# Kernel optimization log

Measured on AMD Instinct MI355X. Metric: run time of the kernel, lower is better.

Reference implementation:

```python
import jax, jax.numpy as jnp
import numpy as np

N, E, M = 100000, 1600000, 10000
D_IN, D_HID, D_OUT = 128, 128, 128


def setup_inputs() -> dict:
    key = jax.random.key(0)
    ks = jax.random.split(key, 16)
    feat = jax.random.normal(ks[0], (N, D_IN), dtype=jnp.float32)
    src = jax.random.randint(ks[1], (E,), 0, N, dtype=jnp.int32)
    dst = jax.random.randint(ks[2], (E,), 0, N, dtype=jnp.int32)
    masked_offset = jax.random.randint(ks[3], (M,), 0, N, dtype=jnp.int32)
    def xavier(k, shape):
        fan_in, fan_out = shape[0], shape[1]
        a = jnp.sqrt(6.0 / (fan_in + fan_out))
        return jax.random.uniform(k, shape, jnp.float32, -a, a)
    return {
        'feat': feat, 'src': src, 'dst': dst, 'masked_offset': masked_offset,
        # GraphConv layers (weight [in,out], bias [out])
        'W1': xavier(ks[4], (D_IN, D_HID)), 'b1': jnp.zeros((D_HID,), jnp.float32),
        'W2': xavier(ks[5], (D_HID, D_HID)), 'b2': jnp.zeros((D_HID,), jnp.float32),
        # fusion MLP
        'Wm1': xavier(ks[6], (D_HID + D_IN, D_HID)), 'bm1': jnp.zeros((D_HID,), jnp.float32),
        'Wm2': xavier(ks[7], (D_HID, D_HID)), 'bm2': jnp.zeros((D_HID,), jnp.float32),
        'Wm3': xavier(ks[8], (D_HID, D_OUT)),  # final Linear has bias=False
    }


def _graph_conv_right(h, src, dst, W, b, inv_deg):
    # DGL GraphConv(norm='right'): aggregate src features at dst, divide by in-degree.
    # Apply weight first (in_feats >= out_feats path) -- mathematically identical.
    hw = h @ W                                   # [N, out]
    agg = jax.ops.segment_sum(hw[src], dst, num_segments=N)  # scatter-add over edges
    return agg * inv_deg + b


def reference(feat, src, dst, masked_offset, W1, b1, W2, b2, Wm1, bm1, Wm2, bm2, Wm3):
    ones = jnp.ones((E,), jnp.float32)
    deg = jax.ops.segment_sum(ones, dst, num_segments=N)
    inv_deg = (1.0 / jnp.clip(deg, 1.0, None))[:, None]      # [N,1]
    # GCN layer 1 + ReLU (Identity norm)
    h = jax.nn.relu(_graph_conv_right(feat, src, dst, W1, b1, inv_deg))
    # GCN layer 2 (last layer: no activation; dropout no-op at eval)
    h = _graph_conv_right(h, src, dst, W2, b2, inv_deg)
    # fusion == 'cat': relu(Identity(h[masked])) concat raw features
    hm = jax.nn.relu(h[masked_offset])                       # [M, H]
    x = jnp.concatenate([hm, feat[masked_offset]], axis=1)   # [M, H+D]
    x = jax.nn.relu(x @ Wm1 + bm1)
    x = jax.nn.relu(x @ Wm2 + bm2)
    return x @ Wm3
```

## Files before the change

### kernel.cpp

```cpp
#include <hip/hip_runtime.h>

#define NN 100000
#define NE 1600000
#define NM 10000
#define NSB 256
#define SUBN 391
#define CAP2 7424
#define PCH 2048

typedef __attribute__((ext_vector_type(8))) short bf16x8;
typedef __attribute__((ext_vector_type(4))) float f32x4;

__device__ inline float4 ld4(const float* p) { return *(const float4*)p; }
__device__ inline float bf2f(unsigned short u) {
  union { unsigned int i; float f; } c; c.i = ((unsigned int)u) << 16; return c.f;
}
__device__ inline unsigned short f2bf(float f) {
  union { float f; unsigned int i; } c; c.f = f;
  unsigned int u = c.i + 0x7fffu + ((c.i >> 16) & 1u);
  return (unsigned short)(u >> 16);
}

__global__ __launch_bounds__(256) void part2_k(const int* __restrict__ src,
                                               const int* __restrict__ dst,
                                               unsigned* __restrict__ parts2,
                                               int* __restrict__ pcnt2) {
  __shared__ int cntw[4][NSB];
  __shared__ int basew[4][NSB];
  __shared__ int bstart[NSB + 1];
  __shared__ int gbase[NSB];
  __shared__ int wsum[4];
  __shared__ unsigned buf[PCH];
  const int tid = threadIdx.x;
  const int wv = tid >> 6;
  const int e0 = blockIdx.x * PCH;

  for (int i = tid; i < 4 * NSB; i += 256) ((int*)cntw)[i] = 0;
  __syncthreads();

  unsigned pk[8];
  int b_[8], lp_[8];
#pragma unroll
  for (int j = 0; j < 8; ++j) {
    int e = e0 + j * 256 + tid;
    bool ok = e < NE;
    int s = ok ? src[e] : 0;
    int d = ok ? dst[e] : 0;
    int b = d / SUBN;
    int ld = d - b * SUBN;
    pk[j] = ((unsigned)ld << 17) | (unsigned)s;
    b_[j] = ok ? b : -1;
    if (ok) lp_[j] = atomicAdd(&cntw[wv][b], 1);
  }
  __syncthreads();
  int t0 = cntw[0][tid], t1 = cntw[1][tid], t2 = cntw[2][tid], t3 = cntw[3][tid];
  int tot = t0 + t1 + t2 + t3;
  int x = tot;
#pragma unroll
  for (int d = 1; d < 64; d <<= 1) {
    int y = __shfl_up(x, d, 64);
    if ((tid & 63) >= d) x += y;
  }
  if ((tid & 63) == 63) wsum[wv] = x;
  __syncthreads();
  int woff = 0;
#pragma unroll
  for (int w = 0; w < 4; ++w) woff += (w < wv) ? wsum[w] : 0;
  int excl = x + woff - tot;
  bstart[tid] = excl;
  basew[0][tid] = excl;
  basew[1][tid] = excl + t0;
  basew[2][tid] = excl + t0 + t1;
  basew[3][tid] = excl + t0 + t1 + t2;
  gbase[tid] = atomicAdd(&pcnt2[tid], tot);
  if (tid == NSB - 1) bstart[NSB] = excl + tot;
  __syncthreads();
#pragma unroll
  for (int j = 0; j < 8; ++j)
    if (b_[j] >= 0) buf[basew[wv][b_[j]] + lp_[j]] = pk[j];
  __syncthreads();
  int total = bstart[NSB];
  for (int i = tid; i < total; i += 256) {
    int lo = 0, hi = NSB;
    while (hi - lo > 1) { int mid = (lo + hi) >> 1; if (bstart[mid] <= i) lo = mid; else hi = mid; }
    int gi = gbase[lo] + (i - bstart[lo]);
    if (gi < CAP2) parts2[(size_t)lo * CAP2 + gi] = buf[i];
  }
}

__global__ __launch_bounds__(1024) void deg2_k(const unsigned* __restrict__ parts2,
                                               const int* __restrict__ pcnt2,
                                               int* __restrict__ deg) {
  __shared__ int cnt[SUBN];
  int sb = blockIdx.x;
  int n = min(pcnt2[sb], CAP2);
  const unsigned* p = parts2 + (size_t)sb * CAP2;
  for (int i = threadIdx.x; i < SUBN; i += 1024) cnt[i] = 0;
  __syncthreads();
  for (int i = threadIdx.x; i < n; i += 1024) atomicAdd(&cnt[p[i] >> 17], 1);
  __syncthreads();
  int base = sb * SUBN;
  for (int i = threadIdx.x; i < SUBN; i += 1024)
    if (base + i < NN) deg[base + i] = cnt[i];
}

__global__ __launch_bounds__(1024) void scan1_k(const int* __restrict__ deg,
                                                int* __restrict__ excl,
                                                int* __restrict__ bsum, int n) {
  __shared__ int lds[1024];
  int tid = threadIdx.x;
  int gid = blockIdx.x * 1024 + tid;
  int v = (gid < n) ? deg[gid] : 0;
  lds[tid] = v;
  __syncthreads();
  for (int off = 1; off < 1024; off <<= 1) {
    int t = (tid >= off) ? lds[tid - off] : 0;
    __syncthreads();
    lds[tid] += t;
    __syncthreads();
  }
  if (gid < n) excl[gid] = lds[tid] - v;
  if (tid == 1023) bsum[blockIdx.x] = lds[1023];
}

__global__ void scan2_k(int* __restrict__ bsum, int nb) {
  __shared__ int lds[128];
  int tid = threadIdx.x;
  int v = (tid < nb) ? bsum[tid] : 0;
  lds[tid] = v;
  __syncthreads();
  for (int off = 1; off < 128; off <<= 1) {
    int t = (tid >= off) ? lds[tid - off] : 0;
    __syncthreads();
    lds[tid] += t;
    __syncthreads();
  }
  if (tid < nb) bsum[tid] = lds[tid] - v;
}

__global__ __launch_bounds__(256) void scan3_k(int* __restrict__ excl,
                                               const int* __restrict__ bsum,
                                               const int* __restrict__ deg,
                                               float* __restrict__ inv, int n) {
  int gid = blockIdx.x * 256 + threadIdx.x;
  if (gid < n) {
    excl[gid] += bsum[gid >> 10] + deg[gid];
    inv[gid] = 1.0f / fmaxf((float)deg[gid], 1.0f);
  }
}

__global__ __launch_bounds__(1024) void sort_emit_k(const unsigned* __restrict__ parts2,
                                                    const int* __restrict__ pcnt2,
                                                    const int* __restrict__ offs_end,
                                                    const int* __restrict__ degv,
                                                    int* __restrict__ csr) {
  __shared__ int cur[SUBN];
  __shared__ int sorted[CAP2];
  int sb = blockIdx.x;
  int n = min(pcnt2[sb], CAP2);
  const unsigned* p = parts2 + (size_t)sb * CAP2;
  int base = sb * SUBN;
  int segbase = offs_end[base] - degv[base];
  for (int i = threadIdx.x; i < SUBN; i += 1024) {
    int nd = base + i;
    cur[i] = (nd < NN) ? (offs_end[nd] - degv[nd]) : 0;
  }
  __syncthreads();
  for (int i = threadIdx.x; i < n; i += 1024) {
    unsigned v = p[i];
    int pos = atomicAdd(&cur[v >> 17], 1);
    sorted[pos - segbase] = (int)(v & 0x1FFFFu);
  }
  __syncthreads();
  for (int i = threadIdx.x; i < n; i += 1024) csr[segbase + i] = sorted[i];
}

__global__ __launch_bounds__(256) void tobf_k(const float* __restrict__ x,
                                              unsigned short* __restrict__ y, int n) {
  int idx = (blockIdx.x * 256 + threadIdx.x) * 4;
  if (idx < n) {
    float4 v = ld4(x + idx);
    unsigned int lo = (unsigned int)f2bf(v.x) | ((unsigned int)f2bf(v.y) << 16);
    unsigned int hi = (unsigned int)f2bf(v.z) | ((unsigned int)f2bf(v.w) << 16);
    *(uint2*)(y + idx) = make_uint2(lo, hi);
  }
}

__device__ inline void conv4(const float* s, unsigned short* d, int q) {
  float4 v = ld4(s + q * 4);
  unsigned int lo = (unsigned int)f2bf(v.x) | ((unsigned int)f2bf(v.y) << 16);
  unsigned int hi = (unsigned int)f2bf(v.z) | ((unsigned int)f2bf(v.w) << 16);
  ((uint2*)d)[q] = make_uint2(lo, hi);
}
__global__ __launch_bounds__(256) void wconv_k(const float* W1, const float* W2,
                                               const float* Wm1, const float* Wm2,
                                               const float* Wm3,
                                               unsigned short* W1bf, unsigned short* W2bf,
                                               unsigned short* Wm1bf, unsigned short* Wm2bf,
                                               unsigned short* Wm3bf) {
  int q = blockIdx.x * 256 + threadIdx.x;
  if (q < 4096) conv4(W1, W1bf, q);
  else if (q < 8192) conv4(W2, W2bf, q - 4096);
  else if (q < 16384) conv4(Wm1, Wm1bf, q - 8192);
  else if (q < 20480) conv4(Wm2, Wm2bf, q - 16384);
  else if (q < 24576) conv4(Wm3, Wm3bf, q - 20480);
}

__global__ __launch_bounds__(256) void gather1_k(const unsigned short* __restrict__ featbf,
                                                 const int* __restrict__ csr,
                                                 const int* __restrict__ offs_end,
                                                 const int* __restrict__ degv,
                                                 const float* __restrict__ inv,
                                                 unsigned short* __restrict__ agg1) {
  int v = blockIdx.x * 8 + (threadIdx.x >> 5);
  if (v >= NN) return;
  int lane = threadIdx.x & 31;
  int cnt = degv[v];
  int start = offs_end[v] - cnt;
  const uint2* fb = (const uint2*)featbf;
  float a0 = 0.f, a1 = 0.f, a2 = 0.f, a3 = 0.f;
  int nb8 = (cnt + 7) >> 3;
  for (int it = 0; it < nb8; ++it) {
    int b = start + (it << 3);
    int rem = cnt - (it << 3);
    int sidx[8]; float msk[8];
#pragma unroll
    for (int j = 0; j < 8; ++j) {
      bool ok = j < rem;
      sidx[j] = csr[b + (ok ? j : 0)];
      msk[j] = ok ? 1.f : 0.f;
    }
    uint2 x[8];
#pragma unroll
    for (int j = 0; j < 8; ++j) x[j] = fb[(size_t)sidx[j] * 32 + lane];
#pragma unroll
    for (int j = 0; j < 8; ++j) {
      a0 = fmaf(msk[j], bf2f((unsigned short)(x[j].x)), a0);
      a1 = fmaf(msk[j], bf2f((unsigned short)(x[j].x >> 16)), a1);
      a2 = fmaf(msk[j], bf2f((unsigned short)(x[j].y)), a2);
      a3 = fmaf(msk[j], bf2f((unsigned short)(x[j].y >> 16)), a3);
    }
  }
  float iv = inv[v];
  unsigned int lo = (unsigned int)f2bf(a0 * iv) | ((unsigned int)f2bf(a1 * iv) << 16);
  unsigned int hi = (unsigned int)f2bf(a2 * iv) | ((unsigned int)f2bf(a3 * iv) << 16);
  ((uint2*)agg1)[(size_t)v * 32 + lane] = make_uint2(lo, hi);
}

__global__ __launch_bounds__(256) void gather2_k(const unsigned short* __restrict__ h1bf,
                                                 const unsigned short* __restrict__ featbf,
                                                 const int* __restrict__ masked,
                                                 const int* __restrict__ csr,
                                                 const int* __restrict__ offs_end,
                                                 const int* __restrict__ degv,
                                                 const float* __restrict__ inv,
                                                 unsigned short* __restrict__ agg2bf,
                                                 unsigned short* __restrict__ xcatbf) {
  int m = blockIdx.x * 8 + (threadIdx.x >> 5);
  if (m >= NM) return;
  int lane = threadIdx.x & 31;
  int v = masked[m];
  int cnt = degv[v];
  int start = offs_end[v] - cnt;
  const uint2* fb = (const uint2*)h1bf;
  float a0 = 0.f, a1 = 0.f, a2 = 0.f, a3 = 0.f;
  int nb8 = (cnt + 7) >> 3;
  for (int it = 0; it < nb8; ++it) {
    int b = start + (it << 3);
    int rem = cnt - (it << 3);
    int sidx[8]; float msk[8];
#pragma unroll
    for (int j = 0; j < 8; ++j) {
      bool ok = j < rem;
      sidx[j] = csr[b + (ok ? j : 0)];
      msk[j] = ok ? 1.f : 0.f;
    }
    uint2 x[8];
#pragma unroll
    for (int j = 0; j < 8; ++j) x[j] = fb[(size_t)sidx[j] * 32 + lane];
#pragma unroll
    for (int j = 0; j < 8; ++j) {
      a0 = fmaf(msk[j], bf2f((unsigned short)(x[j].x)), a0);
      a1 = fmaf(msk[j], bf2f((unsigned short)(x[j].x >> 16)), a1);
      a2 = fmaf(msk[j], bf2f((unsigned short)(x[j].y)), a2);
      a3 = fmaf(msk[j], bf2f((unsigned short)(x[j].y >> 16)), a3);
    }
  }
  float iv = inv[v];
  unsigned int lo = (unsigned int)f2bf(a0 * iv) | ((unsigned int)f2bf(a1 * iv) << 16);
  unsigned int hi = (unsigned int)f2bf(a2 * iv) | ((unsigned int)f2bf(a3 * iv) << 16);
  ((uint2*)agg2bf)[(size_t)m * 32 + lane] = make_uint2(lo, hi);
  ((uint2*)xcatbf)[(size_t)m * 64 + 32 + lane] = ((const uint2*)featbf)[(size_t)v * 32 + lane];
}

template<int KT, bool BIAS, bool RELU, bool F32OUT>
__global__ __launch_bounds__(256) void mfma_gemm_k(const unsigned short* __restrict__ Abf,
                                                   const unsigned short* __restrict__ Wbf,
                                                   const float* __restrict__ bias,
                                                   void* __restrict__ Yout,
                                                   int ldy, int nrows) {
  const int lda = KT * 32;
  const int tid = threadIdx.x;
  const int wave = tid >> 6;
  const int lane = tid & 63;
  const int l15 = lane & 15;
  const int l4 = lane >> 4;
  const int rbase = blockIdx.x * 64;

  bf16x8 Bfr[2][KT];
#pragma unroll
  for (int c = 0; c < 2; ++c) {
    int col = (wave + 4 * c) * 16 + l15;
#pragma unroll
    for (int kt = 0; kt < KT; ++kt) {
      bf16x8 b;
#pragma unroll
      for (int i = 0; i < 8; ++i)
        b[i] = (short)Wbf[(kt * 32 + l4 * 8 + i) * 128 + col];
      Bfr[c][kt] = b;
    }
  }
  float bias0 = 0.f, bias1 = 0.f;
  if (BIAS) { bias0 = bias[wave * 16 + l15]; bias1 = bias[(wave + 4) * 16 + l15]; }

  for (int rsub = 0; rsub < 4; ++rsub) {
    int arow = rbase + rsub * 16 + l15;
    const unsigned short* ap = Abf + (size_t)(arow < nrows ? arow : 0) * lda;
    f32x4 acc0 = {0.f, 0.f, 0.f, 0.f};
    f32x4 acc1 = {0.f, 0.f, 0.f, 0.f};
#pragma unroll
    for (int kt = 0; kt < KT; ++kt) {
      bf16x8 a = *(const bf16x8*)(ap + kt * 32 + l4 * 8);
      acc0 = __builtin_amdgcn_mfma_f32_16x16x32_bf16(a, Bfr[0][kt], acc0, 0, 0, 0);
      acc1 = __builtin_amdgcn_mfma_f32_16x16x32_bf16(a, Bfr[1][kt], acc1, 0, 0, 0);
    }
#pragma unroll
    for (int r = 0; r < 4; ++r) {
      int orow = rbase + rsub * 16 + l4 * 4 + r;
      if (orow < nrows) {
        float v0 = acc0[r] + bias0, v1 = acc1[r] + bias1;
        if (RELU) { v0 = fmaxf(v0, 0.f); v1 = fmaxf(v1, 0.f); }
        if (F32OUT) {
          ((float*)Yout)[(size_t)orow * ldy + wave * 16 + l15] = v0;
          ((float*)Yout)[(size_t)orow * ldy + (wave + 4) * 16 + l15] = v1;
        } else {
          ((unsigned short*)Yout)[(size_t)orow * ldy + wave * 16 + l15] = f2bf(v0);
          ((unsigned short*)Yout)[(size_t)orow * ldy + (wave + 4) * 16 + l15] = f2bf(v1);
        }
      }
    }
  }
}

extern "C" void kernel_launch(void* const* d_in, const int* in_sizes, int n_in,
                              void* d_out, int out_size, void* d_ws, size_t ws_size,
                              hipStream_t stream) {
  const float* feat = (const float*)d_in[0];
  const int* src = (const int*)d_in[1];
  const int* dst = (const int*)d_in[2];
  const int* masked = (const int*)d_in[3];
  const float* W1 = (const float*)d_in[4];
  const float* b1 = (const float*)d_in[5];
  const float* W2 = (const float*)d_in[6];
  const float* b2 = (const float*)d_in[7];
  const float* Wm1 = (const float*)d_in[8];
  const float* bm1 = (const float*)d_in[9];
  const float* Wm2 = (const float*)d_in[10];
  const float* bm2 = (const float*)d_in[11];
  const float* Wm3 = (const float*)d_in[12];
  float* out = (float*)d_out;

  char* p = (char*)d_ws;
  int* deg = (int*)p;              p += (size_t)NN * 4;
  int* offs = (int*)p;             p += (size_t)NN * 4;
  int* bsum = (int*)p;             p += 128 * 4;
  int* pcnt2 = (int*)p;            p += NSB * 4;
  float* inv = (float*)p;          p += (size_t)NN * 4;
  int* csr = (int*)p;              p += (size_t)NE * 4;
  p = (char*)(((size_t)p + 15) & ~(size_t)15);
  unsigned* parts2 = (unsigned*)p; p += (size_t)NSB * CAP2 * 4;
  p = (char*)(((size_t)p + 15) & ~(size_t)15);
  unsigned short* featbf = (unsigned short*)p;  p += (size_t)NN * 128 * 2;
  unsigned short* agg1 = (unsigned short*)p;    p += (size_t)NN * 128 * 2;
  unsigned short* h1bf = (unsigned short*)p;    p += (size_t)NN * 128 * 2;
  unsigned short* W1bf = (unsigned short*)p;    p += 16384 * 2;
  unsigned short* W2bf = (unsigned short*)p;    p += 16384 * 2;
  unsigned short* Wm1bf = (unsigned short*)p;   p += 32768 * 2;
  unsigned short* Wm2bf = (unsigned short*)p;   p += 16384 * 2;
  unsigned short* Wm3bf = (unsigned short*)p;   p += 16384 * 2;
  p = (char*)(((size_t)p + 15) & ~(size_t)15);
  unsigned short* agg2bf = (unsigned short*)p;  p += (size_t)NM * 128 * 2;
  unsigned short* xcatbf = (unsigned short*)p;  p += (size_t)NM * 256 * 2;
  unsigned short* y1bf = (unsigned short*)p;    p += (size_t)NM * 128 * 2;
  unsigned short* y2bf = (unsigned short*)p;    p += (size_t)NM * 128 * 2;

  (void)hipMemsetAsync(pcnt2, 0, NSB * 4, stream);

  part2_k<<<(NE + PCH - 1) / PCH, 256, 0, stream>>>(src, dst, parts2, pcnt2);
  deg2_k<<<NSB, 1024, 0, stream>>>(parts2, pcnt2, deg);
  int nb = (NN + 1023) / 1024;
  scan1_k<<<nb, 1024, 0, stream>>>(deg, offs, bsum, NN);
  scan2_k<<<1, 128, 0, stream>>>(bsum, nb);
  scan3_k<<<(NN + 255) / 256, 256, 0, stream>>>(offs, bsum, deg, inv, NN);
  sort_emit_k<<<NSB, 1024, 0, stream>>>(parts2, pcnt2, offs, deg, csr);

  tobf_k<<<(NN * 128 / 4 + 255) / 256, 256, 0, stream>>>(feat, featbf, NN * 128);
  wconv_k<<<96, 256, 0, stream>>>(W1, W2, Wm1, Wm2, Wm3, W1bf, W2bf, Wm1bf, Wm2bf, Wm3bf);

  gather1_k<<<(NN + 7) / 8, 256, 0, stream>>>(featbf, csr, offs, deg, inv, agg1);
  mfma_gemm_k<4, true, true, false><<<(NN + 63) / 64, 256, 0, stream>>>(agg1, W1bf, b1, h1bf, 128, NN);

  gather2_k<<<(NM + 7) / 8, 256, 0, stream>>>(h1bf, featbf, masked, csr, offs, deg, inv, agg2bf, xcatbf);
  int gm = (NM + 63) / 64;
  mfma_gemm_k<4, true, true, false><<<gm, 256, 0, stream>>>(agg2bf, W2bf, b2, xcatbf, 256, NM);

  mfma_gemm_k<8, true, true, false><<<gm, 256, 0, stream>>>(xcatbf, Wm1bf, bm1, y1bf, 128, NM);
  mfma_gemm_k<4, true, true, false><<<gm, 256, 0, stream>>>(y1bf, Wm2bf, bm2, y2bf, 128, NM);
  mfma_gemm_k<4, false, false, true><<<gm, 256, 0, stream>>>(y2bf, Wm3bf, nullptr, out, 128, NM);
}
```

Before: 181.4 us.

## Skip unneeded layer-1 nodes, fuse gather+GEMM, fuse MLP chain into one kernel

Result: faster. 175.1 us (-3.5%).

```diff
diff --git a/kernel.cpp b/kernel.cpp
--- a/kernel.cpp
+++ b/kernel.cpp
@@ -19,6 +19,15 @@
   union { float f; unsigned int i; } c; c.f = f;
   unsigned int u = c.i + 0x7fffu + ((c.i >> 16) & 1u);
   return (unsigned short)(u >> 16);
+}
+__device__ inline void stx(unsigned char* base, int rowBytes, int row, int col,
+                           unsigned short val) {
+  int bc = col * 2;
+  int c = bc >> 4, cp = c ^ (row & 15);
+  *(unsigned short*)&base[row * rowBytes + (cp << 4) + (bc & 15)] = val;
+}
+__device__ inline bf16x8 ldx8(const unsigned char* base, int rowBytes, int row, int kc) {
+  return *(const bf16x8*)&base[row * rowBytes + ((kc ^ (row & 15)) << 4)];
 }
 
 __global__ __launch_bounds__(256) void part2_k(const int* __restrict__ src,
@@ -31,6 +40,7 @@
   __shared__ int gbase[NSB];
   __shared__ int wsum[4];
   __shared__ unsigned buf[PCH];
+  __shared__ unsigned char bb[PCH];
   const int tid = threadIdx.x;
   const int wv = tid >> 6;
   const int e0 = blockIdx.x * PCH;
@@ -77,14 +87,17 @@
   __syncthreads();
 #pragma unroll
   for (int j = 0; j < 8; ++j)
-    if (b_[j] >= 0) buf[basew[wv][b_[j]] + lp_[j]] = pk[j];
+    if (b_[j] >= 0) {
+      int pos = basew[wv][b_[j]] + lp_[j];
+      buf[pos] = pk[j];
+      bb[pos] = (unsigned char)b_[j];
+    }
   __syncthreads();
   int total = bstart[NSB];
   for (int i = tid; i < total; i += 256) {
-    int lo = 0, hi = NSB;
-    while (hi - lo > 1) { int mid = (lo + hi) >> 1; if (bstart[mid] <= i) lo = mid; else hi = mid; }
-    int gi = gbase[lo] + (i - bstart[lo]);
-    if (gi < CAP2) parts2[(size_t)lo * CAP2 + gi] = buf[i];
+    int b = bb[i];
+    int gi = gbase[b] + (i - bstart[b]);
+    if (gi < CAP2) parts2[(size_t)b * CAP2 + gi] = buf[i];
   }
 }
 
@@ -186,76 +199,128 @@
   }
 }
 
-__device__ inline void conv4(const float* s, unsigned short* d, int q) {
-  float4 v = ld4(s + q * 4);
-  unsigned int lo = (unsigned int)f2bf(v.x) | ((unsigned int)f2bf(v.y) << 16);
-  unsigned int hi = (unsigned int)f2bf(v.z) | ((unsigned int)f2bf(v.w) << 16);
-  ((uint2*)d)[q] = make_uint2(lo, hi);
+__device__ inline void convfrag(const float* W, unsigned short* Wf, int g) {
+  int k8 = (g >> 7) << 3, col = g & 127;
+  unsigned short tmp[8];
+#pragma unroll
+  for (int i = 0; i < 8; ++i) tmp[i] = f2bf(W[(k8 + i) * 128 + col]);
+  *(uint4*)&Wf[(size_t)g * 8] = *(const uint4*)tmp;
 }
 __global__ __launch_bounds__(256) void wconv_k(const float* W1, const float* W2,
                                                const float* Wm1, const float* Wm2,
                                                const float* Wm3,
-                                               unsigned short* W1bf, unsigned short* W2bf,
-                                               unsigned short* Wm1bf, unsigned short* Wm2bf,
-                                               unsigned short* Wm3bf) {
-  int q = blockIdx.x * 256 + threadIdx.x;
-  if (q < 4096) conv4(W1, W1bf, q);
-  else if (q < 8192) conv4(W2, W2bf, q - 4096);
-  else if (q < 16384) conv4(Wm1, Wm1bf, q - 8192);
-  else if (q < 20480) conv4(Wm2, Wm2bf, q - 16384);
-  else if (q < 24576) conv4(Wm3, Wm3bf, q - 20480);
-}
-
-__global__ __launch_bounds__(256) void gather1_k(const unsigned short* __restrict__ featbf,
-                                                 const int* __restrict__ csr,
-                                                 const int* __restrict__ offs_end,
-                                                 const int* __restrict__ degv,
-                                                 const float* __restrict__ inv,
-                                                 unsigned short* __restrict__ agg1) {
-  int v = blockIdx.x * 8 + (threadIdx.x >> 5);
-  if (v >= NN) return;
+                                               unsigned short* W1f, unsigned short* W2f,
+                                               unsigned short* Wm1f, unsigned short* Wm2f,
+                                               unsigned short* Wm3f) {
+  int g = blockIdx.x * 256 + threadIdx.x;
+  if (g < 2048) convfrag(W1, W1f, g);
+  else if (g < 4096) convfrag(W2, W2f, g - 2048);
+  else if (g < 8192) convfrag(Wm1, Wm1f, g - 4096);
+  else if (g < 10240) convfrag(Wm2, Wm2f, g - 8192);
+  else if (g < 12288) convfrag(Wm3, Wm3f, g - 10240);
+}
+
+__global__ __launch_bounds__(256) void mark_k(const int* __restrict__ masked,
+                                              const int* __restrict__ csr,
+                                              const int* __restrict__ offs_end,
+                                              const int* __restrict__ degv,
+                                              unsigned char* __restrict__ needed) {
+  int m = blockIdx.x * 8 + (threadIdx.x >> 5);
+  if (m >= NM) return;
   int lane = threadIdx.x & 31;
+  int v = masked[m];
   int cnt = degv[v];
   int start = offs_end[v] - cnt;
-  const uint2* fb = (const uint2*)featbf;
-  float a0 = 0.f, a1 = 0.f, a2 = 0.f, a3 = 0.f;
-  int nb8 = (cnt + 7) >> 3;
-  for (int it = 0; it < nb8; ++it) {
-    int b = start + (it << 3);
-    int rem = cnt - (it << 3);
-    int sidx[8]; float msk[8];
-#pragma unroll
-    for (int j = 0; j < 8; ++j) {
-      bool ok = j < rem;
-      sidx[j] = csr[b + (ok ? j : 0)];
-      msk[j] = ok ? 1.f : 0.f;
-    }
-    uint2 x[8];
-#pragma unroll
-    for (int j = 0; j < 8; ++j) x[j] = fb[(size_t)sidx[j] * 32 + lane];
-#pragma unroll
-    for (int j = 0; j < 8; ++j) {
-      a0 = fmaf(msk[j], bf2f((unsigned short)(x[j].x)), a0);
-      a1 = fmaf(msk[j], bf2f((unsigned short)(x[j].x >> 16)), a1);
-      a2 = fmaf(msk[j], bf2f((unsigned short)(x[j].y)), a2);
-      a3 = fmaf(msk[j], bf2f((unsigned short)(x[j].y >> 16)), a3);
-    }
-  }
-  float iv = inv[v];
-  unsigned int lo = (unsigned int)f2bf(a0 * iv) | ((unsigned int)f2bf(a1 * iv) << 16);
-  unsigned int hi = (unsigned int)f2bf(a2 * iv) | ((unsigned int)f2bf(a3 * iv) << 16);
-  ((uint2*)agg1)[(size_t)v * 32 + lane] = make_uint2(lo, hi);
+  for (int i = lane; i < cnt; i += 32) needed[csr[start + i]] = 1;
+}
+
+__global__ __launch_bounds__(256) void fused_l1_k(const unsigned short* __restrict__ featbf,
+                                                  const int* __restrict__ csr,
+                                                  const int* __restrict__ offs_end,
+                                                  const int* __restrict__ degv,
+                                                  const float* __restrict__ inv,
+                                                  const unsigned char* __restrict__ needed,
+                                                  const unsigned short* __restrict__ W1f,
+                                                  const float* __restrict__ b1,
+                                                  unsigned short* __restrict__ h1bf) {
+  __shared__ unsigned char lds[64 * 256];
+  const int tid = threadIdx.x;
+  const int rbase = blockIdx.x * 64;
+  {
+    int grp = tid >> 5, lane = tid & 31;
+    const uint2* fb = (const uint2*)featbf;
+    int c = lane >> 1;
+    for (int k = 0; k < 8; ++k) {
+      int row = grp * 8 + k;
+      int v = rbase + row;
+      unsigned char* dstp = &lds[row * 256 + (((c ^ (row & 15)) << 4)) + (lane & 1) * 8];
+      if (v >= NN || !needed[v]) { *(uint2*)dstp = make_uint2(0u, 0u); continue; }
+      int cnt = degv[v];
+      int start = offs_end[v] - cnt;
+      float a0 = 0.f, a1 = 0.f, a2 = 0.f, a3 = 0.f;
+      int nb8 = (cnt + 7) >> 3;
+      for (int it = 0; it < nb8; ++it) {
+        int b = start + (it << 3);
+        int rem = cnt - (it << 3);
+        int sidx[8]; float msk[8];
+#pragma unroll
+        for (int j = 0; j < 8; ++j) {
+          bool ok = j < rem;
+          sidx[j] = csr[b + (ok ? j : 0)];
+          msk[j] = ok ? 1.f : 0.f;
+        }
+        uint2 x[8];
+#pragma unroll
+        for (int j = 0; j < 8; ++j) x[j] = fb[(size_t)sidx[j] * 32 + lane];
+#pragma unroll
+        for (int j = 0; j < 8; ++j) {
+          a0 = fmaf(msk[j], bf2f((unsigned short)(x[j].x)), a0);
+          a1 = fmaf(msk[j], bf2f((unsigned short)(x[j].x >> 16)), a1);
+          a2 = fmaf(msk[j], bf2f((unsigned short)(x[j].y)), a2);
+          a3 = fmaf(msk[j], bf2f((unsigned short)(x[j].y >> 16)), a3);
+        }
+      }
+      float iv = inv[v];
+      unsigned int lo = (unsigned int)f2bf(a0 * iv) | ((unsigned int)f2bf(a1 * iv) << 16);
+      unsigned int hi = (unsigned int)f2bf(a2 * iv) | ((unsigned int)f2bf(a3 * iv) << 16);
+      *(uint2*)dstp = make_uint2(lo, hi);
+    }
+  }
+  __syncthreads();
+  const int wave = tid >> 6, lane = tid & 63, l15 = lane & 15, l4 = lane >> 4;
+  int col0 = wave * 16 + l15, col1 = (wave + 4) * 16 + l15;
+  float bias0 = b1[col0], bias1 = b1[col1];
+  for (int rsub = 0; rsub < 4; ++rsub) {
+    int row = rsub * 16 + l15;
+    f32x4 acc0 = {0.f, 0.f, 0.f, 0.f};
+    f32x4 acc1 = {0.f, 0.f, 0.f, 0.f};
+#pragma unroll
+    for (int kt = 0; kt < 4; ++kt) {
+      int kc = kt * 4 + l4;
+      bf16x8 a = ldx8(lds, 256, row, kc);
+      bf16x8 b0 = *(const bf16x8*)&W1f[((size_t)kc * 128 + col0) * 8];
+      bf16x8 b1v = *(const bf16x8*)&W1f[((size_t)kc * 128 + col1) * 8];
+      acc0 = __builtin_amdgcn_mfma_f32_16x16x32_bf16(a, b0, acc0, 0, 0, 0);
+      acc1 = __builtin_amdgcn_mfma_f32_16x16x32_bf16(a, b1v, acc1, 0, 0, 0);
+    }
+#pragma unroll
+    for (int r = 0; r < 4; ++r) {
+      int orow = rbase + rsub * 16 + l4 * 4 + r;
+      if (orow < NN) {
+        h1bf[(size_t)orow * 128 + col0] = f2bf(fmaxf(acc0[r] + bias0, 0.f));
+        h1bf[(size_t)orow * 128 + col1] = f2bf(fmaxf(acc1[r] + bias1, 0.f));
+      }
+    }
+  }
 }
 
 __global__ __launch_bounds__(256) void gather2_k(const unsigned short* __restrict__ h1bf,
-                                                 const unsigned short* __restrict__ featbf,
                                                  const int* __restrict__ masked,
                                                  const int* __restrict__ csr,
                                                  const int* __restrict__ offs_end,
                                                  const int* __restrict__ degv,
                                                  const float* __restrict__ inv,
-                                                 unsigned short* __restrict__ agg2bf,
-                                                 unsigned short* __restrict__ xcatbf) {
+                                                 unsigned short* __restrict__ agg2bf) {
   int m = blockIdx.x * 8 + (threadIdx.x >> 5);
   if (m >= NM) return;
   int lane = threadIdx.x & 31;
@@ -290,62 +355,140 @@
   unsigned int lo = (unsigned int)f2bf(a0 * iv) | ((unsigned int)f2bf(a1 * iv) << 16);
   unsigned int hi = (unsigned int)f2bf(a2 * iv) | ((unsigned int)f2bf(a3 * iv) << 16);
   ((uint2*)agg2bf)[(size_t)m * 32 + lane] = make_uint2(lo, hi);
-  ((uint2*)xcatbf)[(size_t)m * 64 + 32 + lane] = ((const uint2*)featbf)[(size_t)v * 32 + lane];
-}
-
-template<int KT, bool BIAS, bool RELU, bool F32OUT>
-__global__ __launch_bounds__(256) void mfma_gemm_k(const unsigned short* __restrict__ Abf,
-                                                   const unsigned short* __restrict__ Wbf,
-                                                   const float* __restrict__ bias,
-                                                   void* __restrict__ Yout,
-                                                   int ldy, int nrows) {
-  const int lda = KT * 32;
+}
+
+__global__ __launch_bounds__(256) void mlp_fused_k(const unsigned short* __restrict__ agg2bf,
+                                                   const unsigned short* __restrict__ featbf,
+                                                   const int* __restrict__ masked,
+                                                   const unsigned short* __restrict__ W2f,
+                                                   const float* __restrict__ b2,
+                                                   const unsigned short* __restrict__ Wm1f,
+                                                   const float* __restrict__ bm1,
+                                                   const unsigned short* __restrict__ Wm2f,
+                                                   const float* __restrict__ bm2,
+                                                   const unsigned short* __restrict__ Wm3f,
+                                                   float* __restrict__ out) {
+  __shared__ unsigned char ldsX[64 * 512];
+  __shared__ unsigned char ldsY[64 * 256];
   const int tid = threadIdx.x;
-  const int wave = tid >> 6;
-  const int lane = tid & 63;
-  const int l15 = lane & 15;
-  const int l4 = lane >> 4;
   const int rbase = blockIdx.x * 64;
-
-  bf16x8 Bfr[2][KT];
-#pragma unroll
-  for (int c = 0; c < 2; ++c) {
-    int col = (wave + 4 * c) * 16 + l15;
-#pragma unroll
-    for (int kt = 0; kt < KT; ++kt) {
-      bf16x8 b;
-#pragma unroll
-      for (int i = 0; i < 8; ++i)
-        b[i] = (short)Wbf[(kt * 32 + l4 * 8 + i) * 128 + col];
-      Bfr[c][kt] = b;
-    }
-  }
-  float bias0 = 0.f, bias1 = 0.f;
-  if (BIAS) { bias0 = bias[wave * 16 + l15]; bias1 = bias[(wave + 4) * 16 + l15]; }
-
-  for (int rsub = 0; rsub < 4; ++rsub) {
-    int arow = rbase + rsub * 16 + l15;
-    const unsigned short* ap = Abf + (size_t)(arow < nrows ? arow : 0) * lda;
-    f32x4 acc0 = {0.f, 0.f, 0.f, 0.f};
-    f32x4 acc1 = {0.f, 0.f, 0.f, 0.f};
-#pragma unroll
-    for (int kt = 0; kt < KT; ++kt) {
-      bf16x8 a = *(const bf16x8*)(ap + kt * 32 + l4 * 8);
-      acc0 = __builtin_amdgcn_mfma_f32_16x16x32_bf16(a, Bfr[0][kt], acc0, 0, 0, 0);
-      acc1 = __builtin_amdgcn_mfma_f32_16x16x32_bf16(a, Bfr[1][kt], acc1, 0, 0, 0);
-    }
-#pragma unroll
-    for (int r = 0; r < 4; ++r) {
-      int orow = rbase + rsub * 16 + l4 * 4 + r;
-      if (orow < nrows) {
-        float v0 = acc0[r] + bias0, v1 = acc1[r] + bias1;
-        if (RELU) { v0 = fmaxf(v0, 0.f); v1 = fmaxf(v1, 0.f); }
-        if (F32OUT) {
-          ((float*)Yout)[(size_t)orow * ldy + wave * 16 + l15] = v0;
-          ((float*)Yout)[(size_t)orow * ldy + (wave + 4) * 16 + l15] = v1;
-        } else {
-          ((unsigned short*)Yout)[(size_t)orow * ldy + wave * 16 + l15] = f2bf(v0);
-          ((unsigned short*)Yout)[(size_t)orow * ldy + (wave + 4) * 16 + l15] = f2bf(v1);
+  const int wave = tid >> 6, lane = tid & 63, l15 = lane & 15, l4 = lane >> 4;
+  {
+    int grp = tid >> 5, ln = tid & 31;
+    uint2 vals[8];
+#pragma unroll
+    for (int k = 0; k < 8; ++k) {
+      int m = rbase + grp * 8 + k;
+      vals[k] = make_uint2(0u, 0u);
+      if (m < NM) {
+        int v = masked[m];
+        vals[k] = ((const uint2*)featbf)[(size_t)v * 32 + ln];
+      }
+    }
+#pragma unroll
+    for (int k = 0; k < 8; ++k) {
+      int row = grp * 8 + k;
+      int c = 16 + (ln >> 1);
+      *(uint2*)&ldsX[row * 512 + ((c ^ (row & 15)) << 4) + (ln & 1) * 8] = vals[k];
+    }
+  }
+  {
+    int col0 = wave * 16 + l15, col1 = (wave + 4) * 16 + l15;
+    float bias0 = b2[col0], bias1 = b2[col1];
+    for (int rsub = 0; rsub < 4; ++rsub) {
+      int arow = rbase + rsub * 16 + l15;
+      const unsigned short* ap = agg2bf + (size_t)min(arow, NM - 1) * 128;
+      f32x4 acc0 = {0.f, 0.f, 0.f, 0.f};
+      f32x4 acc1 = {0.f, 0.f, 0.f, 0.f};
+#pragma unroll
+      for (int kt = 0; kt < 4; ++kt) {
+        int kc = kt * 4 + l4;
+        bf16x8 a = *(const bf16x8*)(ap + kc * 8);
+        bf16x8 b0 = *(const bf16x8*)&W2f[((size_t)kc * 128 + col0) * 8];
+        bf16x8 b1v = *(const bf16x8*)&W2f[((size_t)kc * 128 + col1) * 8];
+        acc0 = __builtin_amdgcn_mfma_f32_16x16x32_bf16(a, b0, acc0, 0, 0, 0);
+        acc1 = __builtin_amdgcn_mfma_f32_16x16x32_bf16(a, b1v, acc1, 0, 0, 0);
+      }
+#pragma unroll
+      for (int r = 0; r < 4; ++r) {
+        int row = rsub * 16 + l4 * 4 + r;
+        stx(ldsX, 512, row, col0, f2bf(fmaxf(acc0[r] + bias0, 0.f)));
+        stx(ldsX, 512, row, col1, f2bf(fmaxf(acc1[r] + bias1, 0.f)));
+      }
+    }
+  }
+  __syncthreads();
+  {
+    int col0 = wave * 16 + l15, col1 = (wave + 4) * 16 + l15;
+    float bias0 = bm1[col0], bias1 = bm1[col1];
+    for (int rsub = 0; rsub < 4; ++rsub) {
+      int row = rsub * 16 + l15;
+      f32x4 acc0 = {0.f, 0.f, 0.f, 0.f};
+      f32x4 acc1 = {0.f, 0.f, 0.f, 0.f};
+#pragma unroll
+      for (int kt = 0; kt < 8; ++kt) {
+        int kc = kt * 4 + l4;
+        bf16x8 a = ldx8(ldsX, 512, row, kc);
+        bf16x8 b0 = *(const bf16x8*)&Wm1f[((size_t)kc * 128 + col0) * 8];
+        bf16x8 b1v = *(const bf16x8*)&Wm1f[((size_t)kc * 128 + col1) * 8];
+        acc0 = __builtin_amdgcn_mfma_f32_16x16x32_bf16(a, b0, acc0, 0, 0, 0);
+        acc1 = __builtin_amdgcn_mfma_f32_16x16x32_bf16(a, b1v, acc1, 0, 0, 0);
+      }
+#pragma unroll
+      for (int r = 0; r < 4; ++r) {
+        int row2 = rsub * 16 + l4 * 4 + r;
+        stx(ldsY, 256, row2, col0, f2bf(fmaxf(acc0[r] + bias0, 0.f)));
+        stx(ldsY, 256, row2, col1, f2bf(fmaxf(acc1[r] + bias1, 0.f)));
+      }
+    }
+  }
+  __syncthreads();
+  {
+    int col0 = wave * 16 + l15, col1 = (wave + 4) * 16 + l15;
+    float bias0 = bm2[col0], bias1 = bm2[col1];
+    for (int rsub = 0; rsub < 4; ++rsub) {
+      int row = rsub * 16 + l15;
+      f32x4 acc0 = {0.f, 0.f, 0.f, 0.f};
+      f32x4 acc1 = {0.f, 0.f, 0.f, 0.f};
+#pragma unroll
+      for (int kt = 0; kt < 4; ++kt) {
+        int kc = kt * 4 + l4;
+        bf16x8 a = ldx8(ldsY, 256, row, kc);
+        bf16x8 b0 = *(const bf16x8*)&Wm2f[((size_t)kc * 128 + col0) * 8];
+        bf16x8 b1v = *(const bf16x8*)&Wm2f[((size_t)kc * 128 + col1) * 8];
+        acc0 = __builtin_amdgcn_mfma_f32_16x16x32_bf16(a, b0, acc0, 0, 0, 0);
+        acc1 = __builtin_amdgcn_mfma_f32_16x16x32_bf16(a, b1v, acc1, 0, 0, 0);
+      }
+#pragma unroll
+      for (int r = 0; r < 4; ++r) {
+        int row2 = rsub * 16 + l4 * 4 + r;
+        stx(ldsX, 256, row2, col0, f2bf(fmaxf(acc0[r] + bias0, 0.f)));
+        stx(ldsX, 256, row2, col1, f2bf(fmaxf(acc1[r] + bias1, 0.f)));
+      }
+    }
+  }
+  __syncthreads();
+  {
+    int col0 = wave * 16 + l15, col1 = (wave + 4) * 16 + l15;
+    for (int rsub = 0; rsub < 4; ++rsub) {
+      int row = rsub * 16 + l15;
+      f32x4 acc0 = {0.f, 0.f, 0.f, 0.f};
+      f32x4 acc1 = {0.f, 0.f, 0.f, 0.f};
+#pragma unroll
+      for (int kt = 0; kt < 4; ++kt) {
+        int kc = kt * 4 + l4;
+        bf16x8 a = ldx8(ldsX, 256, row, kc);
+        bf16x8 b0 = *(const bf16x8*)&Wm3f[((size_t)kc * 128 + col0) * 8];
+        bf16x8 b1v = *(const bf16x8*)&Wm3f[((size_t)kc * 128 + col1) * 8];
+        acc0 = __builtin_amdgcn_mfma_f32_16x16x32_bf16(a, b0, acc0, 0, 0, 0);
+        acc1 = __builtin_amdgcn_mfma_f32_16x16x32_bf16(a, b1v, acc1, 0, 0, 0);
+      }
+#pragma unroll
+      for (int r = 0; r < 4; ++r) {
+        int orow = rbase + rsub * 16 + l4 * 4 + r;
+        if (orow < NM) {
+          out[(size_t)orow * 128 + col0] = acc0[r];
+          out[(size_t)orow * 128 + col1] = acc1[r];
         }
       }
     }
@@ -377,24 +520,20 @@
   int* pcnt2 = (int*)p;            p += NSB * 4;
   float* inv = (float*)p;          p += (size_t)NN * 4;
   int* csr = (int*)p;              p += (size_t)NE * 4;
+  unsigned char* needed = (unsigned char*)p; p += (size_t)NN;
   p = (char*)(((size_t)p + 15) & ~(size_t)15);
   unsigned* parts2 = (unsigned*)p; p += (size_t)NSB * CAP2 * 4;
-  p = (char*)(((size_t)p + 15) & ~(size_t)15);
   unsigned short* featbf = (unsigned short*)p;  p += (size_t)NN * 128 * 2;
-  unsigned short* agg1 = (unsigned short*)p;    p += (size_t)NN * 128 * 2;
   unsigned short* h1bf = (unsigned short*)p;    p += (size_t)NN * 128 * 2;
-  unsigned short* W1bf = (unsigned short*)p;    p += 16384 * 2;
-  unsigned short* W2bf = (unsigned short*)p;    p += 16384 * 2;
-  unsigned short* Wm1bf = (unsigned short*)p;   p += 32768 * 2;
-  unsigned short* Wm2bf = (unsigned short*)p;   p += 16384 * 2;
-  unsigned short* Wm3bf = (unsigned short*)p;   p += 16384 * 2;
-  p = (char*)(((size_t)p + 15) & ~(size_t)15);
   unsigned short* agg2bf = (unsigned short*)p;  p += (size_t)NM * 128 * 2;
-  unsigned short* xcatbf = (unsigned short*)p;  p += (size_t)NM * 256 * 2;
-  unsigned short* y1bf = (unsigned short*)p;    p += (size_t)NM * 128 * 2;
-  unsigned short* y2bf = (unsigned short*)p;    p += (size_t)NM * 128 * 2;
+  unsigned short* W1f = (unsigned short*)p;     p += 16384 * 2;
+  unsigned short* W2f = (unsigned short*)p;     p += 16384 * 2;
+  unsigned short* Wm1f = (unsigned short*)p;    p += 32768 * 2;
+  unsigned short* Wm2f = (unsigned short*)p;    p += 16384 * 2;
+  unsigned short* Wm3f = (unsigned short*)p;    p += 16384 * 2;
 
   (void)hipMemsetAsync(pcnt2, 0, NSB * 4, stream);
+  (void)hipMemsetAsync(needed, 0, NN, stream);
 
   part2_k<<<(NE + PCH - 1) / PCH, 256, 0, stream>>>(src, dst, parts2, pcnt2);
   deg2_k<<<NSB, 1024, 0, stream>>>(parts2, pcnt2, deg);
@@ -405,16 +544,14 @@
   sort_emit_k<<<NSB, 1024, 0, stream>>>(parts2, pcnt2, offs, deg, csr);
 
   tobf_k<<<(NN * 128 / 4 + 255) / 256, 256, 0, stream>>>(feat, featbf, NN * 128);
-  wconv_k<<<96, 256, 0, stream>>>(W1, W2, Wm1, Wm2, Wm3, W1bf, W2bf, Wm1bf, Wm2bf, Wm3bf);
-
-  gather1_k<<<(NN + 7) / 8, 256, 0, stream>>>(featbf, csr, offs, deg, inv, agg1);
-  mfma_gemm_k<4, true, true, false><<<(NN + 63) / 64, 256, 0, stream>>>(agg1, W1bf, b1, h1bf, 128, NN);
-
-  gather2_k<<<(NM + 7) / 8, 256, 0, stream>>>(h1bf, featbf, masked, csr, offs, deg, inv, agg2bf, xcatbf);
-  int gm = (NM + 63) / 64;
-  mfma_gemm_k<4, true, true, false><<<gm, 256, 0, stream>>>(agg2bf, W2bf, b2, xcatbf, 256, NM);
-
-  mfma_gemm_k<8, true, true, false><<<gm, 256, 0, stream>>>(xcatbf, Wm1bf, bm1, y1bf, 128, NM);
-  mfma_gemm_k<4, true, true, false><<<gm, 256, 0, stream>>>(y1bf, Wm2bf, bm2, y2bf, 128, NM);
-  mfma_gemm_k<4, false, false, true><<<gm, 256, 0, stream>>>(y2bf, Wm3bf, nullptr, out, 128, NM);
-}
+  wconv_k<<<48, 256, 0, stream>>>(W1, W2, Wm1, Wm2, Wm3, W1f, W2f, Wm1f, Wm2f, Wm3f);
+
+  mark_k<<<(NM + 7) / 8, 256, 0, stream>>>(masked, csr, offs, deg, needed);
+
+  fused_l1_k<<<(NN + 63) / 64, 256, 0, stream>>>(featbf, csr, offs, deg, inv, needed,
+                                                 W1f, b1, h1bf);
+  gather2_k<<<(NM + 7) / 8, 256, 0, stream>>>(h1bf, masked, csr, offs, deg, inv, agg2bf);
+
+  mlp_fused_k<<<(NM + 63) / 64, 256, 0, stream>>>(agg2bf, featbf, masked,
+                                                  W2f, b2, Wm1f, bm1, Wm2f, bm2, Wm3f, out);
+}
```
